# Kernel tuning notes

Measured on AMD Instinct MI355X. Metric: run time of the kernel, lower is better.

Reference implementation:

```python
import jax, jax.numpy as jnp
import numpy as np

B, N, T, F, HID, H = 128, 128, 12, 128, 256, 10


def setup_inputs() -> dict:
    key = jax.random.key(0)
    ks = jax.random.split(key, 8)
    s_in = 1.0 / np.sqrt(F)
    s_hid = 1.0 / np.sqrt(HID)
    return {
        "x": jax.random.normal(ks[0], (B, N, T, F), jnp.float32),
        "adj_weights": jax.random.normal(ks[1], (1, N, N), jnp.float32),
        "W1": jax.random.normal(ks[2], (F, HID), jnp.float32) * s_in,
        "b1": jnp.zeros((HID,), jnp.float32),
        "W2": jax.random.normal(ks[3], (HID, HID), jnp.float32) * s_hid,
        "b2": jnp.zeros((HID,), jnp.float32),
        "W3": jax.random.normal(ks[4], (HID, F), jnp.float32) * s_hid,
        "b3": jnp.zeros((F,), jnp.float32),
    }


def _graph_conv(x, norm_adj, W, b):
    # (B,N,N) @ (B,N,Fin) -> (B,N,Fin), then linear
    h = jnp.einsum("bnm,bmf->bnf", norm_adj, x)
    return h @ W + b


def reference(x, adj_weights, W1, b1, W2, b2, W3, b3):
    # initial state = last time step
    y0 = x[:, :, -1, :]                      # (B,N,F)
    adj = jax.nn.sigmoid(adj_weights)        # (1,N,N)
    adj = jnp.broadcast_to(adj, (x.shape[0], N, N))
    deg = jnp.clip(jnp.sum(adj, axis=-1, keepdims=True), 1.0, None)
    norm_adj = adj / deg                     # degree-normalized adjacency

    def f(y):
        h = jnp.tanh(_graph_conv(y, norm_adj, W1, b1))
        h = jnp.tanh(_graph_conv(h, norm_adj, W2, b2))
        return _graph_conv(h, norm_adj, W3, b3)

    # t = linspace(0, H, H) -> H points, dt = H/(H-1); torchdiffeq 'rk4'
    # uses the 3/8-rule alternative RK4 step (rk4_alt_step_func).
    dt = jnp.float32(H / (H - 1))

    def step(y, _):
        k1 = f(y)
        k2 = f(y + dt * k1 / 3.0)
        k3 = f(y + dt * (k2 - k1 / 3.0))
        k4 = f(y + dt * (k1 - k2 + k3))
        y1 = y + dt * (k1 + 3.0 * (k2 + k3) + k4) / 8.0
        return y1, y1

    _, ys = jax.lax.scan(step, y0, None, length=H - 1)  # (H-1,B,N,F)
    preds = jnp.concatenate([y0[None], ys], axis=0)      # (H,B,N,F)
    return jnp.transpose(preds, (1, 2, 0, 3))            # (B,N,H,F)
```

## Files before the change

### kernel.cpp

```cpp
#include <hip/hip_runtime.h>
#include <hip/hip_bf16.h>

typedef __attribute__((ext_vector_type(8))) short bf16x8;
typedef __attribute__((ext_vector_type(4))) float f32x4;
typedef unsigned short u16;
typedef unsigned int u32;

#define DT_ (10.0f / 9.0f)

__device__ __forceinline__ u16 f2bf(float f) {
  u32 u = __float_as_uint(f);
  u = (u + 0x7FFFu + ((u >> 16) & 1u)) >> 16;
  return (u16)u;
}

__device__ __forceinline__ u32 cvtpk(float lo, float hi) {
  __hip_bfloat162 h = __float22bfloat162_rn(float2{lo, hi});
  return *reinterpret_cast<u32*>(&h);
}

__device__ __forceinline__ float tanh_fast(float x) {
  float ax = fabsf(x);
  float e = __expf(-2.0f * ax);
  float t = (1.0f - e) * __builtin_amdgcn_rcpf(1.0f + e);
  return copysignf(t, x);
}

__device__ __forceinline__ bf16x8 frag_lds(const u16* Mb, int row0, int kE, int strideB) {
  const int l = threadIdx.x & 63;
  const int r = row0 + (l & 15);
  const int kb = (kE + ((l >> 4) << 3)) << 1;
  const int off = r * strideB + (kb ^ ((r & 7) << 4));
  return *(const bf16x8*)((const char*)Mb + off);
}

__device__ __forceinline__ bf16x8 frag_glb(const u16* WT, int col0, int kE, int K) {
  const int l = threadIdx.x & 63;
  const int j = col0 + (l & 15);
  const int k = kE + ((l >> 4) << 3);
  return *(const bf16x8*)(WT + j * K + k);
}

template <int KST, bool BLDS>
__device__ __forceinline__ void gemm2(f32x4 (&acc)[4][2], const u16* Ab, int aStrideB, int mb,
                                      const u16* Bp, int bK, int nb) {
#pragma unroll
  for (int mt = 0; mt < 4; ++mt)
#pragma unroll
    for (int nt = 0; nt < 2; ++nt) acc[mt][nt] = (f32x4){0.f, 0.f, 0.f, 0.f};
  bf16x8 av0[4], bv0[2], av1[4], bv1[2];
#pragma unroll
  for (int nt = 0; nt < 2; ++nt) {
    if constexpr (BLDS) bv0[nt] = frag_lds(Bp, nb + nt * 16, 0, 256);
    else                bv0[nt] = frag_glb(Bp, nb + nt * 16, 0, bK);
  }
#pragma unroll
  for (int mt = 0; mt < 4; ++mt) av0[mt] = frag_lds(Ab, mb + mt * 16, 0, aStrideB);
#pragma unroll 1
  for (int ks = 0; ks < KST; ks += 2) {
    const int k1 = (ks + 1) * 32;
#pragma unroll
    for (int nt = 0; nt < 2; ++nt) {
      if constexpr (BLDS) bv1[nt] = frag_lds(Bp, nb + nt * 16, k1, 256);
      else                bv1[nt] = frag_glb(Bp, nb + nt * 16, k1, bK);
    }
#pragma unroll
    for (int mt = 0; mt < 4; ++mt) av1[mt] = frag_lds(Ab, mb + mt * 16, k1, aStrideB);
#pragma unroll
    for (int nt = 0; nt < 2; ++nt)
#pragma unroll
      for (int mt = 0; mt < 4; ++mt)
        acc[mt][nt] = __builtin_amdgcn_mfma_f32_16x16x32_bf16(av0[mt], bv0[nt], acc[mt][nt], 0, 0, 0);
    if (ks + 2 < KST) {
      const int k2 = (ks + 2) * 32;
#pragma unroll
      for (int nt = 0; nt < 2; ++nt) {
        if constexpr (BLDS) bv0[nt] = frag_lds(Bp, nb + nt * 16, k2, 256);
        else                bv0[nt] = frag_glb(Bp, nb + nt * 16, k2, bK);
      }
#pragma unroll
      for (int mt = 0; mt < 4; ++mt) av0[mt] = frag_lds(Ab, mb + mt * 16, k2, aStrideB);
    }
#pragma unroll
    for (int nt = 0; nt < 2; ++nt)
#pragma unroll
      for (int mt = 0; mt < 4; ++mt)
        acc[mt][nt] = __builtin_amdgcn_mfma_f32_16x16x32_bf16(av1[mt], bv1[nt], acc[mt][nt], 0, 0, 0);
  }
}

template <int KST, bool BLDS>
__device__ __forceinline__ void gemm1(f32x4 (&acc)[4], const u16* Ab, int aStrideB, int mb,
                                      const u16* Bp, int bK, int nb) {
#pragma unroll
  for (int mt = 0; mt < 4; ++mt) acc[mt] = (f32x4){0.f, 0.f, 0.f, 0.f};
  bf16x8 av0[4], av1[4];
  bf16x8 bv0, bv1;
  if constexpr (BLDS) bv0 = frag_lds(Bp, nb, 0, 256);
  else                bv0 = frag_glb(Bp, nb, 0, bK);
#pragma unroll
  for (int mt = 0; mt < 4; ++mt) av0[mt] = frag_lds(Ab, mb + mt * 16, 0, aStrideB);
#pragma unroll 1
  for (int ks = 0; ks < KST; ks += 2) {
    const int k1 = (ks + 1) * 32;
    if constexpr (BLDS) bv1 = frag_lds(Bp, nb, k1, 256);
    else                bv1 = frag_glb(Bp, nb, k1, bK);
#pragma unroll
    for (int mt = 0; mt < 4; ++mt) av1[mt] = frag_lds(Ab, mb + mt * 16, k1, aStrideB);
#pragma unroll
    for (int mt = 0; mt < 4; ++mt)
      acc[mt] = __builtin_amdgcn_mfma_f32_16x16x32_bf16(av0[mt], bv0, acc[mt], 0, 0, 0);
    if (ks + 2 < KST) {
      const int k2 = (ks + 2) * 32;
      if constexpr (BLDS) bv0 = frag_lds(Bp, nb, k2, 256);
      else                bv0 = frag_glb(Bp, nb, k2, bK);
#pragma unroll
      for (int mt = 0; mt < 4; ++mt) av0[mt] = frag_lds(Ab, mb + mt * 16, k2, aStrideB);
    }
#pragma unroll
    for (int mt = 0; mt < 4; ++mt)
      acc[mt] = __builtin_amdgcn_mfma_f32_16x16x32_bf16(av1[mt], bv1, acc[mt], 0, 0, 0);
  }
}

__device__ __forceinline__ void epi_T2(const f32x4 (&acc)[4][2], u16* Q, int nb, int mb, int lane) {
  const int l15 = lane & 15, lg = lane >> 4;
#pragma unroll
  for (int nt = 0; nt < 2; ++nt) {
    const int c = nb + nt * 16 + l15;
    const int swz = (c & 7) << 4;
    char* rowp = (char*)Q + c * 256;
#pragma unroll
    for (int mt = 0; mt < 4; ++mt) {
      f32x4 v = acc[mt][nt];
      const int r0 = mb + mt * 16 + (lg << 2);
      uint2 pk;
      pk.x = cvtpk(v.x, v.y);
      pk.y = cvtpk(v.z, v.w);
      *(uint2*)(rowp + ((r0 << 1) ^ swz)) = pk;
    }
  }
}

__device__ __forceinline__ void epi_N2(const f32x4 (&acc)[4][2], u16* Qlo, int nb, int mb, int lane) {
  const int l15 = lane & 15, lg = lane >> 4;
#pragma unroll
  for (int nt = 0; nt < 2; ++nt) {
    const int c = nb + nt * 16 + l15;
    const int csh = c << 1;
#pragma unroll
    for (int mt = 0; mt < 4; ++mt) {
      f32x4 v = acc[mt][nt];
      const int r0 = mb + mt * 16 + (lg << 2);
      const u32 p01 = cvtpk(v.x, v.y);
      const u32 p23 = cvtpk(v.z, v.w);
      *(u16*)((char*)Qlo + (r0 + 0) * 256 + (csh ^ (((r0 + 0) & 7) << 4))) = (u16)p01;
      *(u16*)((char*)Qlo + (r0 + 1) * 256 + (csh ^ (((r0 + 1) & 7) << 4))) = (u16)(p01 >> 16);
      *(u16*)((char*)Qlo + (r0 + 2) * 256 + (csh ^ (((r0 + 2) & 7) << 4))) = (u16)p23;
      *(u16*)((char*)Qlo + (r0 + 3) * 256 + (csh ^ (((r0 + 3) & 7) << 4))) = (u16)(p23 >> 16);
    }
  }
}

__device__ __forceinline__ void epi_H2(const f32x4 (&acc)[4][2], u16* P, const float* __restrict__ b,
                                       int nb, int mb, int lane) {
  const int l15 = lane & 15, lg = lane >> 4;
#pragma unroll
  for (int nt = 0; nt < 2; ++nt) {
    const int c = nb + nt * 16 + l15;
    const float bb = b[c];
    const int csh = c << 1;
#pragma unroll
    for (int mt = 0; mt < 4; ++mt) {
      f32x4 v = acc[mt][nt];
      const int r0 = mb + mt * 16 + (lg << 2);
      float t0 = tanh_fast(v.x + bb), t1 = tanh_fast(v.y + bb);
      float t2 = tanh_fast(v.z + bb), t3 = tanh_fast(v.w + bb);
      const u32 p01 = cvtpk(t0, t1);
      const u32 p23 = cvtpk(t2, t3);
      *(u16*)((char*)P + (r0 + 0) * 512 + (csh ^ (((r0 + 0) & 7) << 4))) = (u16)p01;
      *(u16*)((char*)P + (r0 + 1) * 512 + (csh ^ (((r0 + 1) & 7) << 4))) = (u16)(p01 >> 16);
      *(u16*)((char*)P + (r0 + 2) * 512 + (csh ^ (((r0 + 2) & 7) << 4))) = (u16)p23;
      *(u16*)((char*)P + (r0 + 3) * 512 + (csh ^ (((r0 + 3) & 7) << 4))) = (u16)(p23 >> 16);
    }
  }
}

template <int E>
__device__ __forceinline__ void feval(int step,
    u16* P, u16* Q, const u16* As,
    const u16* __restrict__ W1T, const u16* __restrict__ W2T, const u16* __restrict__ W3T,
    const float* __restrict__ b1, const float* __restrict__ b2, const float* __restrict__ b3,
    f32x4* __restrict__ SA, f32x4* __restrict__ SB,
    float* __restrict__ out,
    int batch, int tid, int lane, int mb, int wn) {
  const int l15 = lane & 15, lg = lane >> 4;
  u16* Qhi = Q + 16384;

  {
    f32x4 acc[4][2];
    gemm2<4, true>(acc, As, 256, mb, Qhi, 0, wn * 32);
    epi_N2(acc, Q, wn * 32, mb, lane);
  }
  __syncthreads();
#pragma unroll 1
  for (int h = 0; h < 2; ++h) {
    f32x4 acc[4][2];
    gemm2<4, false>(acc, Q, 256, mb, W1T, 128, wn * 64 + h * 32);
    epi_H2(acc, P, b1, wn * 64 + h * 32, mb, lane);
  }
  __syncthreads();
#pragma unroll 1
  for (int h = 0; h < 2; ++h) {
    f32x4 acc[4][2];
    gemm2<8, false>(acc, P, 512, mb, W2T, 256, wn * 64 + h * 32);
    epi_T2(acc, Q, wn * 64 + h * 32, mb, lane);
  }
  __syncthreads();
#pragma unroll 1
  for (int h = 0; h < 2; ++h) {
    f32x4 acc[4][2];
    gemm2<4, true>(acc, As, 256, mb, Q, 0, wn * 64 + h * 32);
    epi_H2(acc, P, b2, wn * 64 + h * 32, mb, lane);
  }
  __syncthreads();
  {
    f32x4 acc[4][2];
    gemm2<8, false>(acc, P, 512, mb, W3T, 256, wn * 32);
    epi_T2(acc, Q, wn * 32, mb, lane);
  }
  __syncthreads();

#pragma unroll 1
  for (int p = 0; p < 2; ++p) {
    f32x4 ya[4], ba[4];
#pragma unroll
    for (int q = 0; q < 4; ++q) ya[q] = SA[(p * 4 + q) * 512 + tid];
    if constexpr (E == 2 || E == 3) {
#pragma unroll
      for (int q = 0; q < 4; ++q) ba[q] = SB[(p * 4 + q) * 512 + tid];
    }
    f32x4 acc[4];
    gemm1<4, true>(acc, As, 256, mb, Q, 0, wn * 32 + p * 16);
    const int c = wn * 32 + p * 16 + l15;
    const float bb = b3[c];
    const int swz = (c & 7) << 4;
    char* zrow = (char*)Qhi + c * 256;
#pragma unroll
    for (int mt = 0; mt < 4; ++mt) {
      f32x4 v = acc[mt];
      const int r0 = mb + mt * 16 + (lg << 2);
      const int i4 = p * 4 + mt;
      f32x4 wa, wb, zv;
#pragma unroll
      for (int e = 0; e < 4; ++e) {
        const int r = r0 + e;
        const float kv = v[e] + bb;
        float z;
        if constexpr (E == 1) {
          wb[e] = kv;
          z = ya[mt][e] + (DT_ * (1.0f / 3.0f)) * kv;
        } else if constexpr (E == 2) {
          const float k1 = ba[mt][e];
          const float y = ya[mt][e];
          z = y + DT_ * (kv - k1 * (1.0f / 3.0f));
          wb[e] = y + DT_ * (k1 - kv);
          wa[e] = y + (DT_ * 0.125f) * (k1 + 3.0f * kv);
        } else if constexpr (E == 3) {
          z = ba[mt][e] + DT_ * kv;
          wa[e] = ya[mt][e] + (DT_ * 0.375f) * kv;
        } else {
          const float yn = ya[mt][e] + (DT_ * 0.125f) * kv;
          wa[e] = yn;
          __builtin_nontemporal_store(yn, &out[batch * 163840 + r * 1280 + (step + 1) * 128 + c]);
          z = yn;
        }
        zv[e] = z;
      }
      uint2 pk;
      pk.x = cvtpk(zv.x, zv.y);
      pk.y = cvtpk(zv.z, zv.w);
      *(uint2*)(zrow + ((r0 << 1) ^ swz)) = pk;
      if constexpr (E == 1 || E == 2) SB[i4 * 512 + tid] = wb;
      if constexpr (E != 1) SA[i4 * 512 + tid] = wa;
    }
  }
  __syncthreads();
}

__global__ __launch_bounds__(512, 2)
void ode_main(
    const u16* __restrict__ Aswz,
    const u16* __restrict__ W1T, const u16* __restrict__ W2T, const u16* __restrict__ W3T,
    const float* __restrict__ b1, const float* __restrict__ b2, const float* __restrict__ b3,
    const float* __restrict__ x,
    f32x4* __restrict__ KS,
    float* __restrict__ out) {
  __shared__ u16 P[32768];
  __shared__ u16 Q[32768];
  __shared__ u16 As[16384];
  const int tid = threadIdx.x;
  const int lane = tid & 63;
  const int wid = tid >> 6;
  const int wm = wid >> 2, wn = wid & 3;
  const int mb = wm * 64;
  const int l15 = lane & 15, lg = lane >> 4;
  const int batch = blockIdx.x;
  f32x4* SA = KS + batch * 8192;
  f32x4* SB = SA + 4096;
  u16* Qhi = Q + 16384;

  {
    const uint4* s = (const uint4*)Aswz;
    uint4* d = (uint4*)As;
#pragma unroll
    for (int i = 0; i < 4; ++i) d[tid + i * 512] = s[tid + i * 512];
  }

#pragma unroll 1
  for (int p = 0; p < 2; ++p)
#pragma unroll 1
    for (int mt = 0; mt < 4; ++mt) {
      const int c = wn * 32 + p * 16 + l15;
      const int r0 = mb + mt * 16 + (lg << 2);
      f32x4 w;
#pragma unroll
      for (int e = 0; e < 4; ++e) {
        const int r = r0 + e;
        const float v = x[((batch * 128 + r) * 12 + 11) * 128 + c];
        w[e] = v;
        __builtin_nontemporal_store(v, &out[batch * 163840 + r * 1280 + c]);
      }
      uint2 pk;
      pk.x = cvtpk(w.x, w.y);
      pk.y = cvtpk(w.z, w.w);
      *(uint2*)((char*)Qhi + c * 256 + ((r0 << 1) ^ ((c & 7) << 4))) = pk;
      SA[(p * 4 + mt) * 512 + tid] = w;
    }
  __syncthreads();

  for (int s = 0; s < 9; ++s) {
    feval<1>(s, P, Q, As, W1T, W2T, W3T, b1, b2, b3, SA, SB, out, batch, tid, lane, mb, wn);
    feval<2>(s, P, Q, As, W1T, W2T, W3T, b1, b2, b3, SA, SB, out, batch, tid, lane, mb, wn);
    feval<3>(s, P, Q, As, W1T, W2T, W3T, b1, b2, b3, SA, SB, out, batch, tid, lane, mb, wn);
    feval<4>(s, P, Q, As, W1T, W2T, W3T, b1, b2, b3, SA, SB, out, batch, tid, lane, mb, wn);
  }
}


__global__ void prep_adj_k(const float* __restrict__ adjw, u16* __restrict__ Aswz) {
  const int n = blockIdx.x;
  const int m = threadIdx.x;
  const float w = adjw[n * 128 + m];
  const float sg = 1.0f / (1.0f + __expf(-w));
  float s = sg;
#pragma unroll
  for (int o = 1; o < 64; o <<= 1) s += __shfl_xor(s, o);
  __shared__ float red[2];
  if ((m & 63) == 0) red[m >> 6] = s;
  __syncthreads();
  const float deg = fmaxf(red[0] + red[1], 1.0f);
  const float v = sg / deg;
  *(u16*)((char*)Aswz + n * 256 + ((m << 1) ^ ((n & 7) << 4))) = f2bf(v);
}

__global__ void prep_w_k(const float* __restrict__ W1, const float* __restrict__ W2,
                         const float* __restrict__ W3,
                         u16* __restrict__ W1T, u16* __restrict__ W2T, u16* __restrict__ W3T) {
  const int i = blockIdx.x * 256 + threadIdx.x;
  if (i < 32768) {
    W1T[i] = f2bf(W1[(i & 127) * 256 + (i >> 7)]);
    W3T[i] = f2bf(W3[(i & 255) * 128 + (i >> 8)]);
  }
  if (i < 65536) W2T[i] = f2bf(W2[(i & 255) * 256 + (i >> 8)]);
}

extern "C" void kernel_launch(void* const* d_in, const int* in_sizes, int n_in,
                              void* d_out, int out_size, void* d_ws, size_t ws_size,
                              hipStream_t stream) {
  const float* x    = (const float*)d_in[0];
  const float* adjw = (const float*)d_in[1];
  const float* W1   = (const float*)d_in[2];
  const float* b1   = (const float*)d_in[3];
  const float* W2   = (const float*)d_in[4];
  const float* b2   = (const float*)d_in[5];
  const float* W3   = (const float*)d_in[6];
  const float* b3   = (const float*)d_in[7];
  float* out = (float*)d_out;

  u16* Aswz = (u16*)d_ws;
  u16* W1T = Aswz + 16384;
  u16* W2T = W1T + 32768;
  u16* W3T = W2T + 65536;
  f32x4* KS = (f32x4*)(W3T + 32768);

  prep_adj_k<<<128, 128, 0, stream>>>(adjw, Aswz);
  prep_w_k<<<256, 256, 0, stream>>>(W1, W2, W3, W1T, W2T, W3T);
  ode_main<<<128, 512, 0, stream>>>(Aswz, W1T, W2T, W3T, b1, b2, b3, x, KS, out);
}
```

Measured before the change: 942.5 us.

## Swap GEMM operand roles so epilogues write packed vector stores instead of scalar

Several GEMMs in the ODE function evaluation now compute the transposed product, with the operands swapped (adjacency or weights as the B side, activations as the A side). Because of this, the epilogues store 8-byte packed bf16 pairs into swizzled LDS rows instead of four scattered 2-byte stores, and the per-row bias is read as a vector. A new gemm2_gA variant reads the weight fragment as A from global memory. The aim is to cut LDS store instruction count and bank conflicts in the epilogues. The risk is that the transposed layouts must stay consistent across every stage that consumes them.

```diff
diff --git a/kernel.cpp b/kernel.cpp
--- a/kernel.cpp
+++ b/kernel.cpp
@@ -34,9 +34,9 @@
   return *(const bf16x8*)((const char*)Mb + off);
 }
 
-__device__ __forceinline__ bf16x8 frag_glb(const u16* WT, int col0, int kE, int K) {
+__device__ __forceinline__ bf16x8 frag_glb(const u16* WT, int row0, int kE, int K) {
   const int l = threadIdx.x & 63;
-  const int j = col0 + (l & 15);
+  const int j = row0 + (l & 15);
   const int k = kE + ((l >> 4) << 3);
   return *(const bf16x8*)(WT + j * K + k);
 }
@@ -89,33 +89,69 @@
   }
 }
 
-template <int KST, bool BLDS>
-__device__ __forceinline__ void gemm1(f32x4 (&acc)[4], const u16* Ab, int aStrideB, int mb,
-                                      const u16* Bp, int bK, int nb) {
+template <int KST>
+__device__ __forceinline__ void gemm2_gA(f32x4 (&acc)[4][2], const u16* Ag, int aK, int mb,
+                                         const u16* Bl, int nb) {
+#pragma unroll
+  for (int mt = 0; mt < 4; ++mt)
+#pragma unroll
+    for (int nt = 0; nt < 2; ++nt) acc[mt][nt] = (f32x4){0.f, 0.f, 0.f, 0.f};
+  bf16x8 av0[4], bv0[2], av1[4], bv1[2];
+#pragma unroll
+  for (int nt = 0; nt < 2; ++nt) bv0[nt] = frag_lds(Bl, nb + nt * 16, 0, 256);
+#pragma unroll
+  for (int mt = 0; mt < 4; ++mt) av0[mt] = frag_glb(Ag, mb + mt * 16, 0, aK);
+#pragma unroll 1
+  for (int ks = 0; ks < KST; ks += 2) {
+    const int k1 = (ks + 1) * 32;
+#pragma unroll
+    for (int nt = 0; nt < 2; ++nt) bv1[nt] = frag_lds(Bl, nb + nt * 16, k1, 256);
+#pragma unroll
+    for (int mt = 0; mt < 4; ++mt) av1[mt] = frag_glb(Ag, mb + mt * 16, k1, aK);
+#pragma unroll
+    for (int nt = 0; nt < 2; ++nt)
+#pragma unroll
+      for (int mt = 0; mt < 4; ++mt)
+        acc[mt][nt] = __builtin_amdgcn_mfma_f32_16x16x32_bf16(av0[mt], bv0[nt], acc[mt][nt], 0, 0, 0);
+    if (ks + 2 < KST) {
+      const int k2 = (ks + 2) * 32;
+#pragma unroll
+      for (int nt = 0; nt < 2; ++nt) bv0[nt] = frag_lds(Bl, nb + nt * 16, k2, 256);
+#pragma unroll
+      for (int mt = 0; mt < 4; ++mt) av0[mt] = frag_glb(Ag, mb + mt * 16, k2, aK);
+    }
+#pragma unroll
+    for (int nt = 0; nt < 2; ++nt)
+#pragma unroll
+      for (int mt = 0; mt < 4; ++mt)
+        acc[mt][nt] = __builtin_amdgcn_mfma_f32_16x16x32_bf16(av1[mt], bv1[nt], acc[mt][nt], 0, 0, 0);
+  }
+}
+
+template <int KST>
+__device__ __forceinline__ void gemm1(f32x4 (&acc)[4], const u16* Ab, int mb,
+                                      const u16* Bp, int nb) {
 #pragma unroll
   for (int mt = 0; mt < 4; ++mt) acc[mt] = (f32x4){0.f, 0.f, 0.f, 0.f};
   bf16x8 av0[4], av1[4];
   bf16x8 bv0, bv1;
-  if constexpr (BLDS) bv0 = frag_lds(Bp, nb, 0, 256);
-  else                bv0 = frag_glb(Bp, nb, 0, bK);
-#pragma unroll
-  for (int mt = 0; mt < 4; ++mt) av0[mt] = frag_lds(Ab, mb + mt * 16, 0, aStrideB);
+  bv0 = frag_lds(Bp, nb, 0, 256);
+#pragma unroll
+  for (int mt = 0; mt < 4; ++mt) av0[mt] = frag_lds(Ab, mb + mt * 16, 0, 256);
 #pragma unroll 1
   for (int ks = 0; ks < KST; ks += 2) {
     const int k1 = (ks + 1) * 32;
-    if constexpr (BLDS) bv1 = frag_lds(Bp, nb, k1, 256);
-    else                bv1 = frag_glb(Bp, nb, k1, bK);
-#pragma unroll
-    for (int mt = 0; mt < 4; ++mt) av1[mt] = frag_lds(Ab, mb + mt * 16, k1, aStrideB);
+    bv1 = frag_lds(Bp, nb, k1, 256);
+#pragma unroll
+    for (int mt = 0; mt < 4; ++mt) av1[mt] = frag_lds(Ab, mb + mt * 16, k1, 256);
 #pragma unroll
     for (int mt = 0; mt < 4; ++mt)
       acc[mt] = __builtin_amdgcn_mfma_f32_16x16x32_bf16(av0[mt], bv0, acc[mt], 0, 0, 0);
     if (ks + 2 < KST) {
       const int k2 = (ks + 2) * 32;
-      if constexpr (BLDS) bv0 = frag_lds(Bp, nb, k2, 256);
-      else                bv0 = frag_glb(Bp, nb, k2, bK);
-#pragma unroll
-      for (int mt = 0; mt < 4; ++mt) av0[mt] = frag_lds(Ab, mb + mt * 16, k2, aStrideB);
+      bv0 = frag_lds(Bp, nb, k2, 256);
+#pragma unroll
+      for (int mt = 0; mt < 4; ++mt) av0[mt] = frag_lds(Ab, mb + mt * 16, k2, 256);
     }
 #pragma unroll
     for (int mt = 0; mt < 4; ++mt)
@@ -123,13 +159,14 @@
   }
 }
 
-__device__ __forceinline__ void epi_T2(const f32x4 (&acc)[4][2], u16* Q, int nb, int mb, int lane) {
+template <int SB>
+__device__ __forceinline__ void epi_U2(const f32x4 (&acc)[4][2], u16* Dst, int nb, int mb, int lane) {
   const int l15 = lane & 15, lg = lane >> 4;
 #pragma unroll
   for (int nt = 0; nt < 2; ++nt) {
     const int c = nb + nt * 16 + l15;
     const int swz = (c & 7) << 4;
-    char* rowp = (char*)Q + c * 256;
+    char* rowp = (char*)Dst + c * SB;
 #pragma unroll
     for (int mt = 0; mt < 4; ++mt) {
       f32x4 v = acc[mt][nt];
@@ -142,46 +179,26 @@
   }
 }
 
-__device__ __forceinline__ void epi_N2(const f32x4 (&acc)[4][2], u16* Qlo, int nb, int mb, int lane) {
+template <int SB>
+__device__ __forceinline__ void epi_U2H(const f32x4 (&acc)[4][2], u16* Dst,
+                                        const float* __restrict__ b, int nb, int mb, int lane) {
   const int l15 = lane & 15, lg = lane >> 4;
 #pragma unroll
   for (int nt = 0; nt < 2; ++nt) {
     const int c = nb + nt * 16 + l15;
-    const int csh = c << 1;
+    const int swz = (c & 7) << 4;
+    char* rowp = (char*)Dst + c * SB;
 #pragma unroll
     for (int mt = 0; mt < 4; ++mt) {
       f32x4 v = acc[mt][nt];
       const int r0 = mb + mt * 16 + (lg << 2);
-      const u32 p01 = cvtpk(v.x, v.y);
-      const u32 p23 = cvtpk(v.z, v.w);
-      *(u16*)((char*)Qlo + (r0 + 0) * 256 + (csh ^ (((r0 + 0) & 7) << 4))) = (u16)p01;
-      *(u16*)((char*)Qlo + (r0 + 1) * 256 + (csh ^ (((r0 + 1) & 7) << 4))) = (u16)(p01 >> 16);
-      *(u16*)((char*)Qlo + (r0 + 2) * 256 + (csh ^ (((r0 + 2) & 7) << 4))) = (u16)p23;
-      *(u16*)((char*)Qlo + (r0 + 3) * 256 + (csh ^ (((r0 + 3) & 7) << 4))) = (u16)(p23 >> 16);
-    }
-  }
-}
-
-__device__ __forceinline__ void epi_H2(const f32x4 (&acc)[4][2], u16* P, const float* __restrict__ b,
-                                       int nb, int mb, int lane) {
-  const int l15 = lane & 15, lg = lane >> 4;
-#pragma unroll
-  for (int nt = 0; nt < 2; ++nt) {
-    const int c = nb + nt * 16 + l15;
-    const float bb = b[c];
-    const int csh = c << 1;
-#pragma unroll
-    for (int mt = 0; mt < 4; ++mt) {
-      f32x4 v = acc[mt][nt];
-      const int r0 = mb + mt * 16 + (lg << 2);
-      float t0 = tanh_fast(v.x + bb), t1 = tanh_fast(v.y + bb);
-      float t2 = tanh_fast(v.z + bb), t3 = tanh_fast(v.w + bb);
-      const u32 p01 = cvtpk(t0, t1);
-      const u32 p23 = cvtpk(t2, t3);
-      *(u16*)((char*)P + (r0 + 0) * 512 + (csh ^ (((r0 + 0) & 7) << 4))) = (u16)p01;
-      *(u16*)((char*)P + (r0 + 1) * 512 + (csh ^ (((r0 + 1) & 7) << 4))) = (u16)(p01 >> 16);
-      *(u16*)((char*)P + (r0 + 2) * 512 + (csh ^ (((r0 + 2) & 7) << 4))) = (u16)p23;
-      *(u16*)((char*)P + (r0 + 3) * 512 + (csh ^ (((r0 + 3) & 7) << 4))) = (u16)(p23 >> 16);
+      const f32x4 bb = *(const f32x4*)(b + r0);
+      float t0 = tanh_fast(v.x + bb.x), t1 = tanh_fast(v.y + bb.y);
+      float t2 = tanh_fast(v.z + bb.z), t3 = tanh_fast(v.w + bb.w);
+      uint2 pk;
+      pk.x = cvtpk(t0, t1);
+      pk.y = cvtpk(t2, t3);
+      *(uint2*)(rowp + ((r0 << 1) ^ swz)) = pk;
     }
   }
 }
@@ -199,35 +216,35 @@
 
   {
     f32x4 acc[4][2];
-    gemm2<4, true>(acc, As, 256, mb, Qhi, 0, wn * 32);
-    epi_N2(acc, Q, wn * 32, mb, lane);
+    gemm2<4, true>(acc, Qhi, 256, mb, As, 0, wn * 32);
+    epi_U2<256>(acc, Q, wn * 32, mb, lane);
   }
   __syncthreads();
 #pragma unroll 1
   for (int h = 0; h < 2; ++h) {
     f32x4 acc[4][2];
-    gemm2<4, false>(acc, Q, 256, mb, W1T, 128, wn * 64 + h * 32);
-    epi_H2(acc, P, b1, wn * 64 + h * 32, mb, lane);
+    gemm2_gA<4>(acc, W1T, 128, h * 128 + mb, Q, wn * 32);
+    epi_U2H<512>(acc, P, b1, wn * 32, h * 128 + mb, lane);
   }
   __syncthreads();
 #pragma unroll 1
   for (int h = 0; h < 2; ++h) {
     f32x4 acc[4][2];
-    gemm2<8, false>(acc, P, 512, mb, W2T, 256, wn * 64 + h * 32);
-    epi_T2(acc, Q, wn * 64 + h * 32, mb, lane);
+    gemm2<8, false>(acc, P, 512, mb, W2T, 256, h * 128 + wn * 32);
+    epi_U2<256>(acc, Q, h * 128 + wn * 32, mb, lane);
   }
   __syncthreads();
 #pragma unroll 1
   for (int h = 0; h < 2; ++h) {
     f32x4 acc[4][2];
-    gemm2<4, true>(acc, As, 256, mb, Q, 0, wn * 64 + h * 32);
-    epi_H2(acc, P, b2, wn * 64 + h * 32, mb, lane);
+    gemm2<4, true>(acc, Q, 256, h * 128 + mb, As, 0, wn * 32);
+    epi_U2H<512>(acc, P, b2, wn * 32, h * 128 + mb, lane);
   }
   __syncthreads();
   {
     f32x4 acc[4][2];
     gemm2<8, false>(acc, P, 512, mb, W3T, 256, wn * 32);
-    epi_T2(acc, Q, wn * 32, mb, lane);
+    epi_U2<256>(acc, Q, wn * 32, mb, lane);
   }
   __syncthreads();
 
@@ -241,7 +258,7 @@
       for (int q = 0; q < 4; ++q) ba[q] = SB[(p * 4 + q) * 512 + tid];
     }
     f32x4 acc[4];
-    gemm1<4, true>(acc, As, 256, mb, Q, 0, wn * 32 + p * 16);
+    gemm1<4>(acc, As, mb, Q, wn * 32 + p * 16);
     const int c = wn * 32 + p * 16 + l15;
     const float bb = b3[c];
     const int swz = (c & 7) << 4;
```

New measurement: 1.022 ms. 1.08x slower.

## Halve waves per block and widen per-wave tiles to 64x64

Applied to the files above, without the earlier changes.

Cuts the block from 8 to 4 waves and gives each wave a 64x64 output tile (4x4 MFMA fragments) instead of 64x32. Larger per-wave tiles raise reuse of A and B fragments, with fewer LDS and global fragment loads per MFMA. The state buffers and epilogues are re-indexed to match. In exchange, per-thread register use roughly doubles and each CU has fewer waves to hide latency.

```diff
diff --git a/kernel.cpp b/kernel.cpp
--- a/kernel.cpp
+++ b/kernel.cpp
@@ -34,23 +34,23 @@
   return *(const bf16x8*)((const char*)Mb + off);
 }
 
-__device__ __forceinline__ bf16x8 frag_glb(const u16* WT, int col0, int kE, int K) {
+__device__ __forceinline__ bf16x8 frag_glb(const u16* WT, int row0, int kE, int K) {
   const int l = threadIdx.x & 63;
-  const int j = col0 + (l & 15);
+  const int j = row0 + (l & 15);
   const int k = kE + ((l >> 4) << 3);
   return *(const bf16x8*)(WT + j * K + k);
 }
 
 template <int KST, bool BLDS>
-__device__ __forceinline__ void gemm2(f32x4 (&acc)[4][2], const u16* Ab, int aStrideB, int mb,
+__device__ __forceinline__ void gemm4(f32x4 (&acc)[4][4], const u16* Ab, int aStrideB, int mb,
                                       const u16* Bp, int bK, int nb) {
 #pragma unroll
   for (int mt = 0; mt < 4; ++mt)
 #pragma unroll
-    for (int nt = 0; nt < 2; ++nt) acc[mt][nt] = (f32x4){0.f, 0.f, 0.f, 0.f};
-  bf16x8 av0[4], bv0[2], av1[4], bv1[2];
-#pragma unroll
-  for (int nt = 0; nt < 2; ++nt) {
+    for (int nt = 0; nt < 4; ++nt) acc[mt][nt] = (f32x4){0.f, 0.f, 0.f, 0.f};
+  bf16x8 av0[4], bv0[4], av1[4], bv1[4];
+#pragma unroll
+  for (int nt = 0; nt < 4; ++nt) {
     if constexpr (BLDS) bv0[nt] = frag_lds(Bp, nb + nt * 16, 0, 256);
     else                bv0[nt] = frag_glb(Bp, nb + nt * 16, 0, bK);
   }
@@ -60,21 +60,21 @@
   for (int ks = 0; ks < KST; ks += 2) {
     const int k1 = (ks + 1) * 32;
 #pragma unroll
-    for (int nt = 0; nt < 2; ++nt) {
+    for (int nt = 0; nt < 4; ++nt) {
       if constexpr (BLDS) bv1[nt] = frag_lds(Bp, nb + nt * 16, k1, 256);
       else                bv1[nt] = frag_glb(Bp, nb + nt * 16, k1, bK);
     }
 #pragma unroll
     for (int mt = 0; mt < 4; ++mt) av1[mt] = frag_lds(Ab, mb + mt * 16, k1, aStrideB);
 #pragma unroll
-    for (int nt = 0; nt < 2; ++nt)
+    for (int nt = 0; nt < 4; ++nt)
 #pragma unroll
       for (int mt = 0; mt < 4; ++mt)
         acc[mt][nt] = __builtin_amdgcn_mfma_f32_16x16x32_bf16(av0[mt], bv0[nt], acc[mt][nt], 0, 0, 0);
     if (ks + 2 < KST) {
       const int k2 = (ks + 2) * 32;
 #pragma unroll
-      for (int nt = 0; nt < 2; ++nt) {
+      for (int nt = 0; nt < 4; ++nt) {
         if constexpr (BLDS) bv0[nt] = frag_lds(Bp, nb + nt * 16, k2, 256);
         else                bv0[nt] = frag_glb(Bp, nb + nt * 16, k2, bK);
       }
@@ -82,54 +82,59 @@
       for (int mt = 0; mt < 4; ++mt) av0[mt] = frag_lds(Ab, mb + mt * 16, k2, aStrideB);
     }
 #pragma unroll
-    for (int nt = 0; nt < 2; ++nt)
+    for (int nt = 0; nt < 4; ++nt)
 #pragma unroll
       for (int mt = 0; mt < 4; ++mt)
         acc[mt][nt] = __builtin_amdgcn_mfma_f32_16x16x32_bf16(av1[mt], bv1[nt], acc[mt][nt], 0, 0, 0);
   }
 }
 
-template <int KST, bool BLDS>
-__device__ __forceinline__ void gemm1(f32x4 (&acc)[4], const u16* Ab, int aStrideB, int mb,
-                                      const u16* Bp, int bK, int nb) {
-#pragma unroll
-  for (int mt = 0; mt < 4; ++mt) acc[mt] = (f32x4){0.f, 0.f, 0.f, 0.f};
-  bf16x8 av0[4], av1[4];
-  bf16x8 bv0, bv1;
-  if constexpr (BLDS) bv0 = frag_lds(Bp, nb, 0, 256);
-  else                bv0 = frag_glb(Bp, nb, 0, bK);
-#pragma unroll
-  for (int mt = 0; mt < 4; ++mt) av0[mt] = frag_lds(Ab, mb + mt * 16, 0, aStrideB);
+template <int KST>
+__device__ __forceinline__ void gemm2L(f32x4 (&acc)[4][2], const u16* Ab, int mb,
+                                       const u16* Bp, int nb) {
+#pragma unroll
+  for (int mt = 0; mt < 4; ++mt)
+#pragma unroll
+    for (int nt = 0; nt < 2; ++nt) acc[mt][nt] = (f32x4){0.f, 0.f, 0.f, 0.f};
+  bf16x8 av0[4], bv0[2], av1[4], bv1[2];
+#pragma unroll
+  for (int nt = 0; nt < 2; ++nt) bv0[nt] = frag_lds(Bp, nb + nt * 16, 0, 256);
+#pragma unroll
+  for (int mt = 0; mt < 4; ++mt) av0[mt] = frag_lds(Ab, mb + mt * 16, 0, 256);
 #pragma unroll 1
   for (int ks = 0; ks < KST; ks += 2) {
     const int k1 = (ks + 1) * 32;
-    if constexpr (BLDS) bv1 = frag_lds(Bp, nb, k1, 256);
-    else                bv1 = frag_glb(Bp, nb, k1, bK);
-#pragma unroll
-    for (int mt = 0; mt < 4; ++mt) av1[mt] = frag_lds(Ab, mb + mt * 16, k1, aStrideB);
-#pragma unroll
-    for (int mt = 0; mt < 4; ++mt)
-      acc[mt] = __builtin_amdgcn_mfma_f32_16x16x32_bf16(av0[mt], bv0, acc[mt], 0, 0, 0);
+#pragma unroll
+    for (int nt = 0; nt < 2; ++nt) bv1[nt] = frag_lds(Bp, nb + nt * 16, k1, 256);
+#pragma unroll
+    for (int mt = 0; mt < 4; ++mt) av1[mt] = frag_lds(Ab, mb + mt * 16, k1, 256);
+#pragma unroll
+    for (int nt = 0; nt < 2; ++nt)
+#pragma unroll
+      for (int mt = 0; mt < 4; ++mt)
+        acc[mt][nt] = __builtin_amdgcn_mfma_f32_16x16x32_bf16(av0[mt], bv0[nt], acc[mt][nt], 0, 0, 0);
     if (ks + 2 < KST) {
       const int k2 = (ks + 2) * 32;
-      if constexpr (BLDS) bv0 = frag_lds(Bp, nb, k2, 256);
-      else                bv0 = frag_glb(Bp, nb, k2, bK);
-#pragma unroll
-      for (int mt = 0; mt < 4; ++mt) av0[mt] = frag_lds(Ab, mb + mt * 16, k2, aStrideB);
-    }
-#pragma unroll
-    for (int mt = 0; mt < 4; ++mt)
-      acc[mt] = __builtin_amdgcn_mfma_f32_16x16x32_bf16(av1[mt], bv1, acc[mt], 0, 0, 0);
-  }
-}
-
-__device__ __forceinline__ void epi_T2(const f32x4 (&acc)[4][2], u16* Q, int nb, int mb, int lane) {
+#pragma unroll
+      for (int nt = 0; nt < 2; ++nt) bv0[nt] = frag_lds(Bp, nb + nt * 16, k2, 256);
+#pragma unroll
+      for (int mt = 0; mt < 4; ++mt) av0[mt] = frag_lds(Ab, mb + mt * 16, k2, 256);
+    }
+#pragma unroll
+    for (int nt = 0; nt < 2; ++nt)
+#pragma unroll
+      for (int mt = 0; mt < 4; ++mt)
+        acc[mt][nt] = __builtin_amdgcn_mfma_f32_16x16x32_bf16(av1[mt], bv1[nt], acc[mt][nt], 0, 0, 0);
+  }
+}
+
+__device__ __forceinline__ void epi_T4(const f32x4 (&acc)[4][4], u16* Dst, int nb, int mb, int lane) {
   const int l15 = lane & 15, lg = lane >> 4;
 #pragma unroll
-  for (int nt = 0; nt < 2; ++nt) {
+  for (int nt = 0; nt < 4; ++nt) {
     const int c = nb + nt * 16 + l15;
     const int swz = (c & 7) << 4;
-    char* rowp = (char*)Q + c * 256;
+    char* rowp = (char*)Dst + c * 256;
 #pragma unroll
     for (int mt = 0; mt < 4; ++mt) {
       f32x4 v = acc[mt][nt];
@@ -142,10 +147,10 @@
   }
 }
 
-__device__ __forceinline__ void epi_N2(const f32x4 (&acc)[4][2], u16* Qlo, int nb, int mb, int lane) {
+__device__ __forceinline__ void epi_N4(const f32x4 (&acc)[4][4], u16* Dst, int nb, int mb, int lane) {
   const int l15 = lane & 15, lg = lane >> 4;
 #pragma unroll
-  for (int nt = 0; nt < 2; ++nt) {
+  for (int nt = 0; nt < 4; ++nt) {
     const int c = nb + nt * 16 + l15;
     const int csh = c << 1;
 #pragma unroll
@@ -154,19 +159,19 @@
       const int r0 = mb + mt * 16 + (lg << 2);
       const u32 p01 = cvtpk(v.x, v.y);
       const u32 p23 = cvtpk(v.z, v.w);
-      *(u16*)((char*)Qlo + (r0 + 0) * 256 + (csh ^ (((r0 + 0) & 7) << 4))) = (u16)p01;
-      *(u16*)((char*)Qlo + (r0 + 1) * 256 + (csh ^ (((r0 + 1) & 7) << 4))) = (u16)(p01 >> 16);
-      *(u16*)((char*)Qlo + (r0 + 2) * 256 + (csh ^ (((r0 + 2) & 7) << 4))) = (u16)p23;
-      *(u16*)((char*)Qlo + (r0 + 3) * 256 + (csh ^ (((r0 + 3) & 7) << 4))) = (u16)(p23 >> 16);
-    }
-  }
-}
-
-__device__ __forceinline__ void epi_H2(const f32x4 (&acc)[4][2], u16* P, const float* __restrict__ b,
+      *(u16*)((char*)Dst + (r0 + 0) * 256 + (csh ^ (((r0 + 0) & 7) << 4))) = (u16)p01;
+      *(u16*)((char*)Dst + (r0 + 1) * 256 + (csh ^ (((r0 + 1) & 7) << 4))) = (u16)(p01 >> 16);
+      *(u16*)((char*)Dst + (r0 + 2) * 256 + (csh ^ (((r0 + 2) & 7) << 4))) = (u16)p23;
+      *(u16*)((char*)Dst + (r0 + 3) * 256 + (csh ^ (((r0 + 3) & 7) << 4))) = (u16)(p23 >> 16);
+    }
+  }
+}
+
+__device__ __forceinline__ void epi_H4(const f32x4 (&acc)[4][4], u16* P, const float* __restrict__ b,
                                        int nb, int mb, int lane) {
   const int l15 = lane & 15, lg = lane >> 4;
 #pragma unroll
-  for (int nt = 0; nt < 2; ++nt) {
+  for (int nt = 0; nt < 4; ++nt) {
     const int c = nb + nt * 16 + l15;
     const float bb = b[c];
     const int csh = c << 1;
@@ -198,97 +203,101 @@
   u16* Qhi = Q + 16384;
 
   {
+    f32x4 acc[4][4];
+    gemm4<4, true>(acc, As, 256, mb, Qhi, 0, wn * 64);
+    epi_N4(acc, Q, wn * 64, mb, lane);
+  }
+  __syncthreads();
+#pragma unroll 1
+  for (int h = 0; h < 2; ++h) {
+    f32x4 acc[4][4];
+    gemm4<4, false>(acc, Q, 256, mb, W1T, 128, h * 128 + wn * 64);
+    epi_H4(acc, P, b1, h * 128 + wn * 64, mb, lane);
+  }
+  __syncthreads();
+#pragma unroll 1
+  for (int h = 0; h < 2; ++h) {
+    f32x4 acc[4][4];
+    gemm4<8, false>(acc, P, 512, mb, W2T, 256, h * 128 + wn * 64);
+    epi_T4(acc, Q, h * 128 + wn * 64, mb, lane);
+  }
+  __syncthreads();
+#pragma unroll 1
+  for (int h = 0; h < 2; ++h) {
+    f32x4 acc[4][4];
+    gemm4<4, true>(acc, As, 256, mb, Q, 0, h * 128 + wn * 64);
+    epi_H4(acc, P, b2, h * 128 + wn * 64, mb, lane);
+  }
+  __syncthreads();
+  {
+    f32x4 acc[4][4];
+    gemm4<8, false>(acc, P, 512, mb, W3T, 256, wn * 64);
+    epi_T4(acc, Q, wn * 64, mb, lane);
+  }
+  __syncthreads();
+
+#pragma unroll 1
+  for (int p = 0; p < 2; ++p) {
+    f32x4 ya[8], ba[8];
+#pragma unroll
+    for (int q = 0; q < 8; ++q) ya[q] = SA[(p * 8 + q) * 256 + tid];
+    if constexpr (E == 2 || E == 3) {
+#pragma unroll
+      for (int q = 0; q < 8; ++q) ba[q] = SB[(p * 8 + q) * 256 + tid];
+    }
     f32x4 acc[4][2];
-    gemm2<4, true>(acc, As, 256, mb, Qhi, 0, wn * 32);
-    epi_N2(acc, Q, wn * 32, mb, lane);
-  }
-  __syncthreads();
-#pragma unroll 1
-  for (int h = 0; h < 2; ++h) {
-    f32x4 acc[4][2];
-    gemm2<4, false>(acc, Q, 256, mb, W1T, 128, wn * 64 + h * 32);
-    epi_H2(acc, P, b1, wn * 64 + h * 32, mb, lane);
-  }
-  __syncthreads();
-#pragma unroll 1
-  for (int h = 0; h < 2; ++h) {
-    f32x4 acc[4][2];
-    gemm2<8, false>(acc, P, 512, mb, W2T, 256, wn * 64 + h * 32);
-    epi_T2(acc, Q, wn * 64 + h * 32, mb, lane);
-  }
-  __syncthreads();
-#pragma unroll 1
-  for (int h = 0; h < 2; ++h) {
-    f32x4 acc[4][2];
-    gemm2<4, true>(acc, As, 256, mb, Q, 0, wn * 64 + h * 32);
-    epi_H2(acc, P, b2, wn * 64 + h * 32, mb, lane);
-  }
-  __syncthreads();
-  {
-    f32x4 acc[4][2];
-    gemm2<8, false>(acc, P, 512, mb, W3T, 256, wn * 32);
-    epi_T2(acc, Q, wn * 32, mb, lane);
-  }
-  __syncthreads();
-
-#pragma unroll 1
-  for (int p = 0; p < 2; ++p) {
-    f32x4 ya[4], ba[4];
-#pragma unroll
-    for (int q = 0; q < 4; ++q) ya[q] = SA[(p * 4 + q) * 512 + tid];
-    if constexpr (E == 2 || E == 3) {
-#pragma unroll
-      for (int q = 0; q < 4; ++q) ba[q] = SB[(p * 4 + q) * 512 + tid];
-    }
-    f32x4 acc[4];
-    gemm1<4, true>(acc, As, 256, mb, Q, 0, wn * 32 + p * 16);
-    const int c = wn * 32 + p * 16 + l15;
-    const float bb = b3[c];
-    const int swz = (c & 7) << 4;
-    char* zrow = (char*)Qhi + c * 256;
-#pragma unroll
-    for (int mt = 0; mt < 4; ++mt) {
-      f32x4 v = acc[mt];
-      const int r0 = mb + mt * 16 + (lg << 2);
-      const int i4 = p * 4 + mt;
-      f32x4 wa, wb, zv;
-#pragma unroll
-      for (int e = 0; e < 4; ++e) {
-        const int r = r0 + e;
-        const float kv = v[e] + bb;
-        float z;
-        if constexpr (E == 1) {
-          wb[e] = kv;
-          z = ya[mt][e] + (DT_ * (1.0f / 3.0f)) * kv;
-        } else if constexpr (E == 2) {
-          const float k1 = ba[mt][e];
-          const float y = ya[mt][e];
-          z = y + DT_ * (kv - k1 * (1.0f / 3.0f));
-          wb[e] = y + DT_ * (k1 - kv);
-          wa[e] = y + (DT_ * 0.125f) * (k1 + 3.0f * kv);
-        } else if constexpr (E == 3) {
-          z = ba[mt][e] + DT_ * kv;
-          wa[e] = ya[mt][e] + (DT_ * 0.375f) * kv;
-        } else {
-          const float yn = ya[mt][e] + (DT_ * 0.125f) * kv;
-          wa[e] = yn;
-          __builtin_nontemporal_store(yn, &out[batch * 163840 + r * 1280 + (step + 1) * 128 + c]);
-          z = yn;
+    gemm2L<4>(acc, As, mb, Q, wn * 64 + p * 32);
+#pragma unroll
+    for (int nt = 0; nt < 2; ++nt) {
+      const int c = wn * 64 + p * 32 + nt * 16 + l15;
+      const float bb = b3[c];
+      const int swz = (c & 7) << 4;
+      char* zrow = (char*)Qhi + c * 256;
+#pragma unroll
+      for (int mt = 0; mt < 4; ++mt) {
+        f32x4 v = acc[mt][nt];
+        const int r0 = mb + mt * 16 + (lg << 2);
+        const int q = mt * 2 + nt;
+        const int i8 = p * 8 + q;
+        f32x4 wa, wb, zv;
+#pragma unroll
+        for (int e = 0; e < 4; ++e) {
+          const int r = r0 + e;
+          const float kv = v[e] + bb;
+          float z;
+          if constexpr (E == 1) {
+            wb[e] = kv;
+            z = ya[q][e] + (DT_ * (1.0f / 3.0f)) * kv;
+          } else if constexpr (E == 2) {
+            const float k1 = ba[q][e];
+            const float y = ya[q][e];
+            z = y + DT_ * (kv - k1 * (1.0f / 3.0f));
+            wb[e] = y + DT_ * (k1 - kv);
+            wa[e] = y + (DT_ * 0.125f) * (k1 + 3.0f * kv);
+          } else if constexpr (E == 3) {
+            z = ba[q][e] + DT_ * kv;
+            wa[e] = ya[q][e] + (DT_ * 0.375f) * kv;
+          } else {
+            const float yn = ya[q][e] + (DT_ * 0.125f) * kv;
+            wa[e] = yn;
+            __builtin_nontemporal_store(yn, &out[batch * 163840 + r * 1280 + (step + 1) * 128 + c]);
+            z = yn;
+          }
+          zv[e] = z;
         }
-        zv[e] = z;
+        uint2 pk;
+        pk.x = cvtpk(zv.x, zv.y);
+        pk.y = cvtpk(zv.z, zv.w);
+        *(uint2*)(zrow + ((r0 << 1) ^ swz)) = pk;
+        if constexpr (E == 1 || E == 2) SB[i8 * 256 + tid] = wb;
+        if constexpr (E != 1) SA[i8 * 256 + tid] = wa;
       }
-      uint2 pk;
-      pk.x = cvtpk(zv.x, zv.y);
-      pk.y = cvtpk(zv.z, zv.w);
-      *(uint2*)(zrow + ((r0 << 1) ^ swz)) = pk;
-      if constexpr (E == 1 || E == 2) SB[i4 * 512 + tid] = wb;
-      if constexpr (E != 1) SA[i4 * 512 + tid] = wa;
-    }
-  }
-  __syncthreads();
-}
-
-__global__ __launch_bounds__(512, 2)
+    }
+  }
+  __syncthreads();
+}
+
+__global__ __launch_bounds__(256, 1)
 void ode_main(
     const u16* __restrict__ Aswz,
     const u16* __restrict__ W1T, const u16* __restrict__ W2T, const u16* __restrict__ W3T,
@@ -302,7 +311,7 @@
   const int tid = threadIdx.x;
   const int lane = tid & 63;
   const int wid = tid >> 6;
-  const int wm = wid >> 2, wn = wid & 3;
+  const int wm = wid >> 1, wn = wid & 1;
   const int mb = wm * 64;
   const int l15 = lane & 15, lg = lane >> 4;
   const int batch = blockIdx.x;
@@ -314,29 +323,31 @@
     const uint4* s = (const uint4*)Aswz;
     uint4* d = (uint4*)As;
 #pragma unroll
-    for (int i = 0; i < 4; ++i) d[tid + i * 512] = s[tid + i * 512];
+    for (int i = 0; i < 8; ++i) d[tid + i * 256] = s[tid + i * 256];
   }
 
 #pragma unroll 1
   for (int p = 0; p < 2; ++p)
 #pragma unroll 1
-    for (int mt = 0; mt < 4; ++mt) {
-      const int c = wn * 32 + p * 16 + l15;
-      const int r0 = mb + mt * 16 + (lg << 2);
-      f32x4 w;
-#pragma unroll
-      for (int e = 0; e < 4; ++e) {
-        const int r = r0 + e;
-        const float v = x[((batch * 128 + r) * 12 + 11) * 128 + c];
-        w[e] = v;
-        __builtin_nontemporal_store(v, &out[batch * 163840 + r * 1280 + c]);
+    for (int mt = 0; mt < 4; ++mt)
+#pragma unroll 1
+      for (int nt = 0; nt < 2; ++nt) {
+        const int c = wn * 64 + p * 32 + nt * 16 + l15;
+        const int r0 = mb + mt * 16 + (lg << 2);
+        f32x4 w;
+#pragma unroll
+        for (int e = 0; e < 4; ++e) {
+          const int r = r0 + e;
+          const float v = x[((batch * 128 + r) * 12 + 11) * 128 + c];
+          w[e] = v;
+          __builtin_nontemporal_store(v, &out[batch * 163840 + r * 1280 + c]);
+        }
+        uint2 pk;
+        pk.x = cvtpk(w.x, w.y);
+        pk.y = cvtpk(w.z, w.w);
+        *(uint2*)((char*)Qhi + c * 256 + ((r0 << 1) ^ ((c & 7) << 4))) = pk;
+        SA[(p * 8 + mt * 2 + nt) * 256 + tid] = w;
       }
-      uint2 pk;
-      pk.x = cvtpk(w.x, w.y);
-      pk.y = cvtpk(w.z, w.w);
-      *(uint2*)((char*)Qhi + c * 256 + ((r0 << 1) ^ ((c & 7) << 4))) = pk;
-      SA[(p * 4 + mt) * 512 + tid] = w;
-    }
   __syncthreads();
 
   for (int s = 0; s < 9; ++s) {
@@ -396,5 +407,5 @@
 
   prep_adj_k<<<128, 128, 0, stream>>>(adjw, Aswz);
   prep_w_k<<<256, 256, 0, stream>>>(W1, W2, W3, W1T, W2T, W3T);
-  ode_main<<<128, 512, 0, stream>>>(Aswz, W1T, W2T, W3T, b1, b2, b3, x, KS, out);
-}
+  ode_main<<<128, 256, 0, stream>>>(Aswz, W1T, W2T, W3T, b1, b2, b3, x, KS, out);
+}
```

After: 1.229 ms. 1.3x slower.

## Retile weight GEMMs to 32x128 warp tiles reusing global weight fragments

Applied to the files above, without the earlier changes.

Replaces the 64x32 per-warp tiles (looped twice) of the W1 and W2 weight GEMMs with one 32x128 tile per warp. Each warp now loads 8 weight fragments from global memory per k-step and reuses them across two row tiles, so fewer A fragments are read from LDS and the h-loop overhead goes away. The adjacency GEMM column mapping is reordered to interleave warps across the two 128-column halves. The cost is higher register pressure from 16 accumulators and 8 B fragments, and the software double-buffering used by the old path is dropped.

```diff
diff --git a/kernel.cpp b/kernel.cpp
--- a/kernel.cpp
+++ b/kernel.cpp
@@ -34,9 +34,9 @@
   return *(const bf16x8*)((const char*)Mb + off);
 }
 
-__device__ __forceinline__ bf16x8 frag_glb(const u16* WT, int col0, int kE, int K) {
+__device__ __forceinline__ bf16x8 frag_glb(const u16* WT, int row0, int kE, int K) {
   const int l = threadIdx.x & 63;
-  const int j = col0 + (l & 15);
+  const int j = row0 + (l & 15);
   const int k = kE + ((l >> 4) << 3);
   return *(const bf16x8*)(WT + j * K + k);
 }
@@ -89,33 +89,54 @@
   }
 }
 
-template <int KST, bool BLDS>
-__device__ __forceinline__ void gemm1(f32x4 (&acc)[4], const u16* Ab, int aStrideB, int mb,
-                                      const u16* Bp, int bK, int nb) {
+template <int KST>
+__device__ __forceinline__ void gemmW(f32x4 (&acc)[2][8], const u16* Ab, int aStrideB, int mb,
+                                      const u16* WT, int bK, int nb) {
+#pragma unroll
+  for (int mt = 0; mt < 2; ++mt)
+#pragma unroll
+    for (int nt = 0; nt < 8; ++nt) acc[mt][nt] = (f32x4){0.f, 0.f, 0.f, 0.f};
+#pragma unroll 1
+  for (int ks = 0; ks < KST; ++ks) {
+    const int kE = ks * 32;
+    bf16x8 bv[8];
+#pragma unroll
+    for (int nt = 0; nt < 8; ++nt) bv[nt] = frag_glb(WT, nb + nt * 16, kE, bK);
+    bf16x8 av[2];
+#pragma unroll
+    for (int mt = 0; mt < 2; ++mt) av[mt] = frag_lds(Ab, mb + mt * 16, kE, aStrideB);
+#pragma unroll
+    for (int nt = 0; nt < 8; ++nt)
+#pragma unroll
+      for (int mt = 0; mt < 2; ++mt)
+        acc[mt][nt] = __builtin_amdgcn_mfma_f32_16x16x32_bf16(av[mt], bv[nt], acc[mt][nt], 0, 0, 0);
+  }
+}
+
+template <int KST>
+__device__ __forceinline__ void gemm1(f32x4 (&acc)[4], const u16* Ab, int mb,
+                                      const u16* Bp, int nb) {
 #pragma unroll
   for (int mt = 0; mt < 4; ++mt) acc[mt] = (f32x4){0.f, 0.f, 0.f, 0.f};
   bf16x8 av0[4], av1[4];
   bf16x8 bv0, bv1;
-  if constexpr (BLDS) bv0 = frag_lds(Bp, nb, 0, 256);
-  else                bv0 = frag_glb(Bp, nb, 0, bK);
-#pragma unroll
-  for (int mt = 0; mt < 4; ++mt) av0[mt] = frag_lds(Ab, mb + mt * 16, 0, aStrideB);
+  bv0 = frag_lds(Bp, nb, 0, 256);
+#pragma unroll
+  for (int mt = 0; mt < 4; ++mt) av0[mt] = frag_lds(Ab, mb + mt * 16, 0, 256);
 #pragma unroll 1
   for (int ks = 0; ks < KST; ks += 2) {
     const int k1 = (ks + 1) * 32;
-    if constexpr (BLDS) bv1 = frag_lds(Bp, nb, k1, 256);
-    else                bv1 = frag_glb(Bp, nb, k1, bK);
-#pragma unroll
-    for (int mt = 0; mt < 4; ++mt) av1[mt] = frag_lds(Ab, mb + mt * 16, k1, aStrideB);
+    bv1 = frag_lds(Bp, nb, k1, 256);
+#pragma unroll
+    for (int mt = 0; mt < 4; ++mt) av1[mt] = frag_lds(Ab, mb + mt * 16, k1, 256);
 #pragma unroll
     for (int mt = 0; mt < 4; ++mt)
       acc[mt] = __builtin_amdgcn_mfma_f32_16x16x32_bf16(av0[mt], bv0, acc[mt], 0, 0, 0);
     if (ks + 2 < KST) {
       const int k2 = (ks + 2) * 32;
-      if constexpr (BLDS) bv0 = frag_lds(Bp, nb, k2, 256);
-      else                bv0 = frag_glb(Bp, nb, k2, bK);
-#pragma unroll
-      for (int mt = 0; mt < 4; ++mt) av0[mt] = frag_lds(Ab, mb + mt * 16, k2, aStrideB);
+      bv0 = frag_lds(Bp, nb, k2, 256);
+#pragma unroll
+      for (int mt = 0; mt < 4; ++mt) av0[mt] = frag_lds(Ab, mb + mt * 16, k2, 256);
     }
 #pragma unroll
     for (int mt = 0; mt < 4; ++mt)
@@ -142,7 +163,26 @@
   }
 }
 
-__device__ __forceinline__ void epi_N2(const f32x4 (&acc)[4][2], u16* Qlo, int nb, int mb, int lane) {
+__device__ __forceinline__ void epi_TW(const f32x4 (&acc)[2][8], u16* Q, int nb, int mb, int lane) {
+  const int l15 = lane & 15, lg = lane >> 4;
+#pragma unroll
+  for (int nt = 0; nt < 8; ++nt) {
+    const int c = nb + nt * 16 + l15;
+    const int swz = (c & 7) << 4;
+    char* rowp = (char*)Q + c * 256;
+#pragma unroll
+    for (int mt = 0; mt < 2; ++mt) {
+      f32x4 v = acc[mt][nt];
+      const int r0 = mb + mt * 16 + (lg << 2);
+      uint2 pk;
+      pk.x = cvtpk(v.x, v.y);
+      pk.y = cvtpk(v.z, v.w);
+      *(uint2*)(rowp + ((r0 << 1) ^ swz)) = pk;
+    }
+  }
+}
+
+__device__ __forceinline__ void epi_N2(const f32x4 (&acc)[4][2], u16* Dst, int nb, int mb, int lane) {
   const int l15 = lane & 15, lg = lane >> 4;
 #pragma unroll
   for (int nt = 0; nt < 2; ++nt) {
@@ -154,10 +194,10 @@
       const int r0 = mb + mt * 16 + (lg << 2);
       const u32 p01 = cvtpk(v.x, v.y);
       const u32 p23 = cvtpk(v.z, v.w);
-      *(u16*)((char*)Qlo + (r0 + 0) * 256 + (csh ^ (((r0 + 0) & 7) << 4))) = (u16)p01;
-      *(u16*)((char*)Qlo + (r0 + 1) * 256 + (csh ^ (((r0 + 1) & 7) << 4))) = (u16)(p01 >> 16);
-      *(u16*)((char*)Qlo + (r0 + 2) * 256 + (csh ^ (((r0 + 2) & 7) << 4))) = (u16)p23;
-      *(u16*)((char*)Qlo + (r0 + 3) * 256 + (csh ^ (((r0 + 3) & 7) << 4))) = (u16)(p23 >> 16);
+      *(u16*)((char*)Dst + (r0 + 0) * 256 + (csh ^ (((r0 + 0) & 7) << 4))) = (u16)p01;
+      *(u16*)((char*)Dst + (r0 + 1) * 256 + (csh ^ (((r0 + 1) & 7) << 4))) = (u16)(p01 >> 16);
+      *(u16*)((char*)Dst + (r0 + 2) * 256 + (csh ^ (((r0 + 2) & 7) << 4))) = (u16)p23;
+      *(u16*)((char*)Dst + (r0 + 3) * 256 + (csh ^ (((r0 + 3) & 7) << 4))) = (u16)(p23 >> 16);
     }
   }
 }
@@ -186,6 +226,30 @@
   }
 }
 
+__device__ __forceinline__ void epi_HW(const f32x4 (&acc)[2][8], u16* P, const float* __restrict__ b,
+                                       int nb, int mb, int lane) {
+  const int l15 = lane & 15, lg = lane >> 4;
+#pragma unroll
+  for (int nt = 0; nt < 8; ++nt) {
+    const int c = nb + nt * 16 + l15;
+    const float bb = b[c];
+    const int csh = c << 1;
+#pragma unroll
+    for (int mt = 0; mt < 2; ++mt) {
+      f32x4 v = acc[mt][nt];
+      const int r0 = mb + mt * 16 + (lg << 2);
+      float t0 = tanh_fast(v.x + bb), t1 = tanh_fast(v.y + bb);
+      float t2 = tanh_fast(v.z + bb), t3 = tanh_fast(v.w + bb);
+      const u32 p01 = cvtpk(t0, t1);
+      const u32 p23 = cvtpk(t2, t3);
+      *(u16*)((char*)P + (r0 + 0) * 512 + (csh ^ (((r0 + 0) & 7) << 4))) = (u16)p01;
+      *(u16*)((char*)P + (r0 + 1) * 512 + (csh ^ (((r0 + 1) & 7) << 4))) = (u16)(p01 >> 16);
+      *(u16*)((char*)P + (r0 + 2) * 512 + (csh ^ (((r0 + 2) & 7) << 4))) = (u16)p23;
+      *(u16*)((char*)P + (r0 + 3) * 512 + (csh ^ (((r0 + 3) & 7) << 4))) = (u16)(p23 >> 16);
+    }
+  }
+}
+
 template <int E>
 __device__ __forceinline__ void feval(int step,
     u16* P, u16* Q, const u16* As,
@@ -195,6 +259,9 @@
     float* __restrict__ out,
     int batch, int tid, int lane, int mb, int wn) {
   const int l15 = lane & 15, lg = lane >> 4;
+  const int wid = tid >> 6;
+  const int mbW = (wid >> 1) * 32;
+  const int cbW = (wid & 1) * 128;
   u16* Qhi = Q + 16384;
 
   {
@@ -203,25 +270,23 @@
     epi_N2(acc, Q, wn * 32, mb, lane);
   }
   __syncthreads();
+  {
+    f32x4 acc[2][8];
+    gemmW<4>(acc, Q, 256, mbW, W1T, 128, cbW);
+    epi_HW(acc, P, b1, cbW, mbW, lane);
+  }
+  __syncthreads();
+  {
+    f32x4 acc[2][8];
+    gemmW<8>(acc, P, 512, mbW, W2T, 256, cbW);
+    epi_TW(acc, Q, cbW, mbW, lane);
+  }
+  __syncthreads();
 #pragma unroll 1
   for (int h = 0; h < 2; ++h) {
     f32x4 acc[4][2];
-    gemm2<4, false>(acc, Q, 256, mb, W1T, 128, wn * 64 + h * 32);
-    epi_H2(acc, P, b1, wn * 64 + h * 32, mb, lane);
-  }
-  __syncthreads();
-#pragma unroll 1
-  for (int h = 0; h < 2; ++h) {
-    f32x4 acc[4][2];
-    gemm2<8, false>(acc, P, 512, mb, W2T, 256, wn * 64 + h * 32);
-    epi_T2(acc, Q, wn * 64 + h * 32, mb, lane);
-  }
-  __syncthreads();
-#pragma unroll 1
-  for (int h = 0; h < 2; ++h) {
-    f32x4 acc[4][2];
-    gemm2<4, true>(acc, As, 256, mb, Q, 0, wn * 64 + h * 32);
-    epi_H2(acc, P, b2, wn * 64 + h * 32, mb, lane);
+    gemm2<4, true>(acc, As, 256, mb, Q, 0, h * 128 + wn * 32);
+    epi_H2(acc, P, b2, h * 128 + wn * 32, mb, lane);
   }
   __syncthreads();
   {
@@ -241,7 +306,7 @@
       for (int q = 0; q < 4; ++q) ba[q] = SB[(p * 4 + q) * 512 + tid];
     }
     f32x4 acc[4];
-    gemm1<4, true>(acc, As, 256, mb, Q, 0, wn * 32 + p * 16);
+    gemm1<4>(acc, As, mb, Q, wn * 32 + p * 16);
     const int c = wn * 32 + p * 16 + l15;
     const float bb = b3[c];
     const int swz = (c & 7) << 4;
```

Result: slower. 1.546 ms (+64.0%).
